# Performance work log

Hardware: AMD Instinct MI355X
Metric: run time of the kernel (lower is better)

## Reference

```python
import jax, jax.numpy as jnp
import numpy as np

N = 4096
NHID = 256
K1, K2, K3 = 3072, 2304, 1728


def _layernorm(x, g, b, eps=1e-5):
    m = jnp.mean(x, axis=-1, keepdims=True)
    v = jnp.mean((x - m) ** 2, axis=-1, keepdims=True)
    return (x - m) / jnp.sqrt(v + eps) * g + b


def _gcn(x, A, W, b):
    # PyG GCNConv: add self loops, symmetric norm D^-1/2 (A+I) D^-1/2,
    # messages flow row(source) -> col(target): out[j] = sum_i Anorm[i,j] (xW)[i] + b
    n = A.shape[0]
    A_sl = A + jnp.eye(n, dtype=A.dtype)
    deg = A_sl.sum(0)  # in-degree over col index incl. self loop
    dinv = jnp.where(deg > 0, deg ** -0.5, 0.0)
    An = A_sl * dinv[:, None] * dinv[None, :]
    return An.T @ (x @ W) + b


def _sagpool(x, A, Wp, bp, k):
    score = jnp.tanh(_gcn(x, A, Wp, bp)[:, 0])  # [n]
    vals, perm = jax.lax.top_k(score, k)
    x_new = x[perm] * vals[:, None]
    A_new = A[perm][:, perm]  # induced subgraph of directed edges
    return x_new, A_new


def _readout(x):
    # cat([global_max_pool, global_mean_pool]) for a single graph -> [1, 2*nhid]
    return jnp.concatenate([x.max(0), x.mean(0)])[None, :]


def setup_inputs() -> dict:
    key = jax.random.key(0)
    ks = jax.random.split(key, 10)
    s = 0.05
    return {
        'feature': jax.random.normal(ks[0], (N, 500), jnp.float32),
        'img_info': jax.random.normal(ks[1], (N, 6), jnp.float32),
        'Wp': jax.random.normal(ks[2], (6, 12), jnp.float32) * s,
        'bp': jnp.zeros((12,), jnp.float32),
        'ln_f_g': jnp.ones((500,), jnp.float32),
        'ln_f_b': jnp.zeros((500,), jnp.float32),
        'ln_p_g': jnp.ones((12,), jnp.float32),
        'ln_p_b': jnp.zeros((12,), jnp.float32),
        'W1': jax.random.normal(ks[3], (512, NHID), jnp.float32) * s,
        'b1': jnp.zeros((NHID,), jnp.float32),
        'Wpool1': jax.random.normal(ks[4], (NHID, 1), jnp.float32) * s,
        'bpool1': jnp.zeros((1,), jnp.float32),
        'W2': jax.random.normal(ks[5], (NHID, NHID), jnp.float32) * s,
        'b2': jnp.zeros((NHID,), jnp.float32),
        'Wpool2': jax.random.normal(ks[6], (NHID, 1), jnp.float32) * s,
        'bpool2': jnp.zeros((1,), jnp.float32),
        'W3': jax.random.normal(ks[7], (NHID, NHID), jnp.float32) * s,
        'b3': jnp.zeros((NHID,), jnp.float32),
        'Wpool3': jax.random.normal(ks[8], (NHID, 1), jnp.float32) * s,
        'bpool3': jnp.zeros((1,), jnp.float32),
    }


def reference(feature, img_info, Wp, bp, ln_f_g, ln_f_b, ln_p_g, ln_p_b,
              W1, b1, Wpool1, bpool1, W2, b2, Wpool2, bpool2,
              W3, b3, Wpool3, bpool3):
    # pos embedding + self-attention over nodes
    pos = img_info @ Wp + bp                                  # [N,12]
    att = jax.nn.softmax(pos @ pos.T / jnp.sqrt(12.0), axis=1)  # [N,N]
    pos = att @ pos

    f = _layernorm(feature, ln_f_g, ln_f_b)
    p = _layernorm(pos, ln_p_g, ln_p_b)
    x0 = jnp.concatenate([f, p], axis=1)                      # [N,512]

    # edge construction: upper-triangular directed edges where sqdist < 0.5*max sqdist
    sq = jnp.sum(x0 * x0, axis=1)
    d2 = sq[:, None] - 2.0 * (x0 @ x0.T) + sq[None, :]        # [N,N]
    t = 0.5 * d2.max()
    n = x0.shape[0]
    iu = jnp.triu(jnp.ones((n, n), bool), 1)
    A = jnp.where((d2 < t) & iu, 1.0, 0.0).astype(x0.dtype)

    x = jax.nn.relu(_gcn(x0, A, W1, b1))
    x, A = _sagpool(x, A, Wpool1, bpool1, K1)
    x1 = _readout(x)

    x = jax.nn.relu(_gcn(x, A, W2, b2))
    x, A = _sagpool(x, A, Wpool2, bpool2, K2)
    x2 = _readout(x)

    x = jax.nn.relu(_gcn(x, A, W3, b3))
    x, A = _sagpool(x, A, Wpool3, bpool3, K3)
    x3 = _readout(x)

    return x1 + x2 + x3  # [1, 512]
```

## Files before the change

### kernel.cpp

```cpp
#include <hip/hip_runtime.h>
#include <math.h>

#define NN 4096
#define RB 128

typedef __attribute__((ext_vector_type(8))) short bf16x8;
typedef __attribute__((ext_vector_type(4))) float f32x4;

__device__ __forceinline__ unsigned encf(float f) {
  unsigned u = __float_as_uint(f);
  return (u & 0x80000000u) ? ~u : (u | 0x80000000u);
}
__device__ __forceinline__ float decf(unsigned u) {
  return __uint_as_float((u & 0x80000000u) ? (u ^ 0x80000000u) : ~u);
}
__device__ __forceinline__ unsigned short f2bf(float f) {
  unsigned u = __float_as_uint(f);
  return (unsigned short)((u + 0x7fffu + ((u >> 16) & 1u)) >> 16);
}

__global__ void k_pos(const float* img, const float* Wp, const float* bp, float* pos,
                      float* out, unsigned* dmax) {
  if (blockIdx.x == 0) {
    int tt = threadIdx.x;
    out[tt] = 0.f; out[256 + tt] = 0.f;
    if (tt == 0) *dmax = 0u;
  }
  int t = blockIdx.x * 256 + threadIdx.x;
  if (t >= NN * 12) return;
  int i = t / 12, d = t % 12;
  float s = bp[d];
#pragma unroll
  for (int k = 0; k < 6; ++k) s += img[i * 6 + k] * Wp[k * 12 + d];
  pos[t] = s;
}

__global__ __launch_bounds__(256) void k_attn3(const float* pos, float* out) {
  __shared__ float sp[12][256];
  int t = threadIdx.x, lane = t & 63, w = t >> 6;
  int ib = blockIdx.x * 8 + w * 2;
  float pi[2][12];
#pragma unroll
  for (int r = 0; r < 2; ++r)
#pragma unroll
    for (int d = 0; d < 12; ++d) pi[r][d] = pos[(ib + r) * 12 + d] * 0.28867513459481287f;
  float sl[2] = {0.f, 0.f};
  float acc[2][12] = {};
  const float4* p4 = (const float4*)pos;
  for (int kt = 0; kt < NN; kt += 256) {
    __syncthreads();
    int j = kt + t;
    float4 a = p4[j * 3 + 0], b = p4[j * 3 + 1], c = p4[j * 3 + 2];
    sp[0][t] = a.x; sp[1][t] = a.y; sp[2][t] = a.z; sp[3][t] = a.w;
    sp[4][t] = b.x; sp[5][t] = b.y; sp[6][t] = b.z; sp[7][t] = b.w;
    sp[8][t] = c.x; sp[9][t] = c.y; sp[10][t] = c.z; sp[11][t] = c.w;
    __syncthreads();
#pragma unroll
    for (int q = 0; q < 4; ++q) {
      int jj = q * 64 + lane;
      float pj[12];
#pragma unroll
      for (int d = 0; d < 12; ++d) pj[d] = sp[d][jj];
#pragma unroll
      for (int r = 0; r < 2; ++r) {
        float s = 0.f;
#pragma unroll
        for (int d = 0; d < 12; ++d) s = fmaf(pi[r][d], pj[d], s);
        float e = __expf(s);
        sl[r] += e;
#pragma unroll
        for (int d = 0; d < 12; ++d) acc[r][d] = fmaf(e, pj[d], acc[r][d]);
      }
    }
  }
#pragma unroll
  for (int r = 0; r < 2; ++r) {
    float s = sl[r];
#pragma unroll
    for (int o = 32; o > 0; o >>= 1) s += __shfl_xor(s, o);
    float ad[12];
#pragma unroll
    for (int d = 0; d < 12; ++d) {
      ad[d] = acc[r][d];
#pragma unroll
      for (int o = 32; o > 0; o >>= 1) ad[d] += __shfl_xor(ad[d], o);
    }
    if (lane == 0) {
      float inv = 1.f / s;
#pragma unroll
      for (int d = 0; d < 12; ++d) out[(ib + r) * 12 + d] = ad[d] * inv;
    }
  }
}

__global__ __launch_bounds__(256) void k_lnx(const float* f, const float* g, const float* b,
                                             const float* p, const float* pg, const float* pb,
                                             float* x0, unsigned short* x0h, float* sqv,
                                             int* degA) {
  __shared__ float row[512];
  __shared__ float wrA[4], wrB[4], wrC[4];
  int i = blockIdx.x, t = threadIdx.x, lane = t & 63, w = t >> 6;
  if (t == 0) degA[i] = 0;
  float v1 = f[i * 500 + t];
  float v2 = (t < 244) ? f[i * 500 + 256 + t] : 0.f;
  float part = v1 + v2;
#pragma unroll
  for (int o = 32; o > 0; o >>= 1) part += __shfl_xor(part, o);
  if (lane == 0) wrA[w] = part;
  __syncthreads();
  float m = (wrA[0] + wrA[1] + wrA[2] + wrA[3]) * (1.f / 500.f);
  float d1 = v1 - m, d2 = v2 - m;
  float pvv = d1 * d1 + ((t < 244) ? d2 * d2 : 0.f);
#pragma unroll
  for (int o = 32; o > 0; o >>= 1) pvv += __shfl_xor(pvv, o);
  if (lane == 0) wrB[w] = pvv;
  __syncthreads();
  float scale = 1.f / sqrtf((wrB[0] + wrB[1] + wrB[2] + wrB[3]) * (1.f / 500.f) + 1e-5f);
  row[t] = d1 * scale * g[t] + b[t];
  if (t < 244) row[256 + t] = d2 * scale * g[256 + t] + b[256 + t];
  if (t >= 244) {
    int tt = t - 244;
    float pv[12], pm = 0.f;
#pragma unroll
    for (int d = 0; d < 12; ++d) { pv[d] = p[i * 12 + d]; pm += pv[d]; }
    pm *= (1.f / 12.f);
    float pvar = 0.f;
#pragma unroll
    for (int d = 0; d < 12; ++d) { float dd = pv[d] - pm; pvar += dd * dd; }
    pvar *= (1.f / 12.f);
    float ps = 1.f / sqrtf(pvar + 1e-5f);
    row[500 + tt] = (pv[tt] - pm) * ps * pg[tt] + pb[tt];
  }
  __syncthreads();
  float a = row[t], c = row[256 + t];
  float sq = a * a + c * c;
#pragma unroll
  for (int o = 32; o > 0; o >>= 1) sq += __shfl_xor(sq, o);
  if (lane == 0) wrC[w] = sq;
  __syncthreads();
  if (t == 0) sqv[i] = wrC[0] + wrC[1] + wrC[2] + wrC[3];
  x0[(size_t)i * 512 + t] = a;
  x0[(size_t)i * 512 + 256 + t] = c;
  x0h[(size_t)i * 512 + t] = f2bf(a);
  x0h[(size_t)i * 512 + 256 + t] = f2bf(c);
}

#define BK 64
template <bool MASK>
__global__ __launch_bounds__(256) void k_d2m(const unsigned short* X, const float* sqv,
                                             unsigned* dmax, float* tileMin,
                                             unsigned char* ATm, int* deg) {
  __shared__ unsigned short As[2][128 * BK];
  __shared__ unsigned short Bs[2][128 * BK];
  __shared__ float wmax[4], wmin[4];
  const int NT = NN / 128;
  int bid0 = blockIdx.x;
  int bid = (bid0 & 7) * 66 + (bid0 >> 3);
  int ti = 0, rem = bid;
  while (rem >= NT - ti) { rem -= NT - ti; ++ti; }
  int tj = ti + rem;
  int t = threadIdx.x, lane = t & 63, w = t >> 6;
  int wr = w >> 1, wc = w & 1;
  const unsigned short* Abase = X + (size_t)ti * 128 * 512;
  const unsigned short* Bbase = X + (size_t)tj * 128 * 512;
  int lr = lane >> 3, lc = lane & 7;

  float thr = 0.f;
  if (MASK) {
    thr = 0.5f * decf(*dmax);
    uint4 z = make_uint4(0u, 0u, 0u, 0u);
    if (ti != tj) {
#pragma unroll
      for (int q0 = 0; q0 < 4; ++q0) {
        int q = t + q0 * 256; int r = q >> 3, c4 = q & 7;
        *(uint4*)(ATm + (size_t)(ti * 128 + r) * NN + tj * 128 + c4 * 16) = z;
      }
    }
    if (tileMin[blockIdx.x] >= thr) {
#pragma unroll
      for (int q0 = 0; q0 < 4; ++q0) {
        int q = t + q0 * 256; int r = q >> 3, c4 = q & 7;
        *(uint4*)(ATm + (size_t)(tj * 128 + r) * NN + ti * 128 + c4 * 16) = z;
      }
      return;
    }
  }

  auto stage = [&](int buf, int k0) {
#pragma unroll
    for (int i = 0; i < 4; ++i) {
      int q = w * 4 + i;
      int r = q * 8 + lr;
      int cs = lc ^ (r & 7);
      __builtin_amdgcn_global_load_lds(
          (const __attribute__((address_space(1))) unsigned int*)(Abase + (size_t)r * 512 + k0 + cs * 8),
          (__attribute__((address_space(3))) unsigned int*)(&As[buf][q * 512]), 16, 0, 0);
      __builtin_amdgcn_global_load_lds(
          (const __attribute__((address_space(1))) unsigned int*)(Bbase + (size_t)r * 512 + k0 + cs * 8),
          (__attribute__((address_space(3))) unsigned int*)(&Bs[buf][q * 512]), 16, 0, 0);
    }
  };

  stage(0, 0);

  f32x4 acc[4][4] = {};
  int rl = lane & 15, kg = lane >> 4;
  for (int step = 0; step < 8; ++step) {
    int cur = step & 1;
    if (step < 7) {
      stage(cur ^ 1, (step + 1) * BK);
      asm volatile("s_waitcnt vmcnt(8)" ::: "memory");
    } else {
      asm volatile("s_waitcnt vmcnt(0)" ::: "memory");
    }
    __builtin_amdgcn_sched_barrier(0);
    __builtin_amdgcn_s_barrier();
#pragma unroll
    for (int ks = 0; ks < 2; ++ks) {
      bf16x8 af[4], bq[4];
#pragma unroll
      for (int f = 0; f < 4; ++f) {
        int rA = wr * 64 + f * 16 + rl;
        af[f] = *(const bf16x8*)(&As[cur][rA * BK + (((ks * 4 + kg) ^ (rA & 7)) << 3)]);
        int rB = wc * 64 + f * 16 + rl;
        bq[f] = *(const bf16x8*)(&Bs[cur][rB * BK + (((ks * 4 + kg) ^ (rB & 7)) << 3)]);
      }
#pragma unroll
      for (int a = 0; a < 4; ++a)
#pragma unroll
        for (int b = 0; b < 4; ++b)
          acc[a][b] = __builtin_amdgcn_mfma_f32_16x16x32_bf16(af[a], bq[b], acc[a][b], 0, 0, 0);
    }
    __builtin_amdgcn_sched_barrier(0);
    __builtin_amdgcn_s_barrier();
  }
  int rbase = ti * 128 + wr * 64 + ((lane >> 4) << 2);
  int cbase = tj * 128 + wc * 64 + (lane & 15);
  if (!MASK) {
    float lm = -1e30f, lmin = 1e30f;
#pragma unroll
    for (int a = 0; a < 4; ++a) {
      float si[4];
#pragma unroll
      for (int r = 0; r < 4; ++r) si[r] = sqv[rbase + a * 16 + r];
#pragma unroll
      for (int b = 0; b < 4; ++b) {
        int gj = cbase + b * 16;
        float sj = sqv[gj];
#pragma unroll
        for (int r = 0; r < 4; ++r) {
          float d2v = si[r] - 2.f * acc[a][b][r] + sj;
          lm = fmaxf(lm, d2v);
          if (rbase + a * 16 + r < gj) lmin = fminf(lmin, d2v);
        }
      }
    }
#pragma unroll
    for (int o = 32; o > 0; o >>= 1) {
      lm = fmaxf(lm, __shfl_xor(lm, o));
      lmin = fminf(lmin, __shfl_xor(lmin, o));
    }
    if (lane == 0) { wmax[w] = lm; wmin[w] = lmin; }
    __syncthreads();
    if (t == 0) {
      atomicMax(dmax, encf(fmaxf(fmaxf(wmax[0], wmax[1]), fmaxf(wmax[2], wmax[3]))));
      tileMin[blockIdx.x] = fminf(fminf(wmin[0], wmin[1]), fminf(wmin[2], wmin[3]));
    }
  } else {
#pragma unroll
    for (int b = 0; b < 4; ++b) {
      int gj = cbase + b * 16;
      float sj = sqv[gj];
      int rowcnt = 0;
#pragma unroll
      for (int a = 0; a < 4; ++a) {
        int gi0 = rbase + a * 16;
        union { unsigned char c[4]; unsigned u; } m4;
#pragma unroll
        for (int r = 0; r < 4; ++r) {
          float d2v = sqv[gi0 + r] - 2.f * acc[a][b][r] + sj;
          unsigned char mv = (d2v < thr && (gi0 + r) < gj) ? 1 : 0;
          m4.c[r] = mv; rowcnt += mv;
        }
        *(unsigned*)(ATm + (size_t)gj * NN + gi0) = m4.u;
      }
      if (rowcnt) atomicAdd(&deg[gj], rowcnt);
    }
  }
}

__global__ __launch_bounds__(256) void k_gemm(const float* A, const float* B, const int* deg,
                                              float* C, int M, int N, int K) {
  __shared__ float Ast[16][34];
  __shared__ float Bs[16][64];
  int t = threadIdx.x, tx = t & 15, ty = t >> 4;
  int nbx = N >> 6;
  int total = gridDim.x;
  int bid0 = blockIdx.x;
  int bid = (bid0 & 7) * (total >> 3) + (bid0 >> 3);
  int m0 = (bid / nbx) * 32, n0 = (bid % nbx) * 64;
  int ar = t >> 3, ac = (t * 2) & 15;
  int br = t >> 4, bc = (t & 15) * 4;
  float2 ra = *(const float2*)(A + (size_t)(m0 + ar) * K + ac);
  float4 rb = *(const float4*)(B + (size_t)br * N + n0 + bc);
  float acc[2][4] = {};
  for (int k0 = 0; k0 < K; k0 += 16) {
    Ast[ac][ar] = ra.x; Ast[ac + 1][ar] = ra.y;
    *(float4*)(&Bs[br][bc]) = rb;
    __syncthreads();
    if (k0 + 16 < K) {
      ra = *(const float2*)(A + (size_t)(m0 + ar) * K + k0 + 16 + ac);
      rb = *(const float4*)(B + (size_t)(k0 + 16 + br) * N + n0 + bc);
    }
#pragma unroll
    for (int kk = 0; kk < 16; ++kk) {
      float2 av = *(const float2*)(&Ast[kk][ty * 2]);
      float4 bv = *(const float4*)(&Bs[kk][tx * 4]);
      acc[0][0] = fmaf(av.x, bv.x, acc[0][0]);
      acc[0][1] = fmaf(av.x, bv.y, acc[0][1]);
      acc[0][2] = fmaf(av.x, bv.z, acc[0][2]);
      acc[0][3] = fmaf(av.x, bv.w, acc[0][3]);
      acc[1][0] = fmaf(av.y, bv.x, acc[1][0]);
      acc[1][1] = fmaf(av.y, bv.y, acc[1][1]);
      acc[1][2] = fmaf(av.y, bv.z, acc[1][2]);
      acc[1][3] = fmaf(av.y, bv.w, acc[1][3]);
    }
    __syncthreads();
  }
#pragma unroll
  for (int a = 0; a < 2; ++a) {
    float dv = 1.f / sqrtf((float)(1 + deg[m0 + ty * 2 + a]));
#pragma unroll
    for (int b2 = 0; b2 < 4; ++b2)
      C[(size_t)(m0 + ty * 2 + a) * N + n0 + tx * 4 + b2] = acc[a][b2] * dv;
  }
}

__global__ __launch_bounds__(256) void k_agg(const float* y, const unsigned char* ATm,
                                             const int* deg, const float* bias,
                                             const float* Wpool, float* out, float* y2, int n) {
  __shared__ unsigned char mrow[256];
  __shared__ int s_any;
  __shared__ float wred[4];
  int j = blockIdx.x, t = threadIdx.x, lane = t & 63, w = t >> 6;
  int dg = deg[j];
  float dj = 1.f / sqrtf((float)(1 + dg));
  float acc = y[(size_t)j * 256 + t];
  if (dg != 0) {
    for (int i0 = 0; i0 < n; i0 += 256) {
      if (t == 0) s_any = 0;
      __syncthreads();
      unsigned char m = ATm[(size_t)j * n + i0 + t];
      mrow[t] = m;
      if (m) s_any = 1;
      __syncthreads();
      if (s_any) {
        for (int u = 0; u < 256; ++u)
          if (mrow[u]) acc += y[(size_t)(i0 + u) * 256 + t];
      }
      __syncthreads();
    }
  }
  float o = fmaxf(dj * acc + bias[t], 0.f);
  out[(size_t)j * 256 + t] = o;
  float rv = o * Wpool[t];
#pragma unroll
  for (int os = 32; os > 0; os >>= 1) rv += __shfl_xor(rv, os);
  if (lane == 0) wred[w] = rv;
  __syncthreads();
  if (t == 0) y2[j] = dj * (wred[0] + wred[1] + wred[2] + wred[3]);
}

__global__ __launch_bounds__(256) void k_scorek(const float* y2, const unsigned char* ATm,
                                                const int* deg, const float* bp,
                                                float* score, int n) {
  int w = threadIdx.x >> 6, lane = threadIdx.x & 63;
  int j = blockIdx.x * 4 + w;
  if (j >= n) return;
  int dg = deg[j];
  float dj = 1.f / sqrtf((float)(1 + dg));
  float s = 0.f;
  if (dg != 0) {
    const uint4* row = (const uint4*)(ATm + (size_t)j * n);
    for (int p = lane; p < n / 16; p += 64) {
      uint4 v = row[p];
      if (v.x | v.y | v.z | v.w) {
        int base = p * 16;
#pragma unroll
        for (int q = 0; q < 4; ++q) {
          unsigned u = (&v.x)[q];
#pragma unroll
          for (int b2 = 0; b2 < 4; ++b2)
            if ((u >> (8 * b2)) & 0xffu) s += y2[base + q * 4 + b2];
        }
      }
    }
    for (int sh = 32; sh > 0; sh >>= 1) s += __shfl_down(s, sh);
  }
  if (lane == 0) score[j] = tanhf(dj * (y2[j] + s) + bp[0]);
}

__global__ __launch_bounds__(1024) void k_topsel(const float* score, int n, int k,
                                                 int* perm, float* vals) {
  __shared__ unsigned keys[4096];
  __shared__ unsigned hist[256];
  __shared__ unsigned s_state[2];
  __shared__ unsigned woff[16];
  int t = threadIdx.x, lane = t & 63, w = t >> 6;
  for (int i = t; i < 4096; i += 1024) keys[i] = (i < n) ? encf(score[i]) : 0u;
  if (t == 0) { s_state[0] = 0u; s_state[1] = (unsigned)k; }
  __syncthreads();

  for (int pass = 0; pass < 4; ++pass) {
    int shift = 24 - pass * 8;
    if (t < 256) hist[t] = 0u;
    __syncthreads();
    unsigned prefix = s_state[0];
    unsigned need = s_state[1];
    unsigned pmask = pass ? (0xFFFFFFFFu << (shift + 8)) : 0u;
    for (int i = t; i < n; i += 1024) {
      unsigned kk = keys[i];
      if ((kk & pmask) == prefix) atomicAdd(&hist[(kk >> shift) & 255u], 1u);
    }
    __syncthreads();
    if (w == 0) {
      unsigned h[4], suf[4];
#pragma unroll
      for (int r = 0; r < 4; ++r) h[r] = hist[lane * 4 + r];
      suf[3] = h[3]; suf[2] = h[2] + suf[3]; suf[1] = h[1] + suf[2]; suf[0] = h[0] + suf[1];
      unsigned lsum = suf[0];
      unsigned s = lsum;
#pragma unroll
      for (int off = 1; off < 64; off <<= 1) {
        unsigned o = __shfl_down(s, off);
        if (lane + off < 64) s += o;
      }
      unsigned Hl = s - lsum;
      int cand = -1; unsigned cumAt = 0, histAt = 0;
#pragma unroll
      for (int r = 0; r < 4; ++r) {
        unsigned c = Hl + suf[r];
        if (c >= need) { cand = lane * 4 + r; cumAt = c; histAt = h[r]; }
      }
      int gmax = cand;
#pragma unroll
      for (int off = 32; off > 0; off >>= 1) {
        int o = __shfl_xor(gmax, off);
        gmax = o > gmax ? o : gmax;
      }
      if (cand == gmax && cand >= 0) {
        s_state[0] = prefix | ((unsigned)cand << shift);
        s_state[1] = need - (cumAt - histAt);
      }
    }
    __syncthreads();
  }
  unsigned cutoff = s_state[0];
  unsigned tcount = s_state[1];
  unsigned G = (unsigned)k - tcount;

  int i0 = t * 4;
  unsigned loc[4], cnt = 0;
#pragma unroll
  for (int r = 0; r < 4; ++r) {
    unsigned kk = keys[i0 + r];
    unsigned g = (kk > cutoff) ? 1u : 0u;
    unsigned e = (kk == cutoff) ? 1u : 0u;
    loc[r] = cnt;
    cnt += (g << 16) | e;
  }
  unsigned inc = cnt;
#pragma unroll
  for (int off = 1; off < 64; off <<= 1) {
    unsigned o = __shfl_up(inc, off);
    if (lane >= off) inc += o;
  }
  if (lane == 63) woff[w] = inc;
  __syncthreads();
  if (t == 0) {
    unsigned run = 0;
    for (int q = 0; q < 16; ++q) { unsigned v = woff[q]; woff[q] = run; run += v; }
  }
  __syncthreads();
  unsigned base = woff[w] + (inc - cnt);
#pragma unroll
  for (int r = 0; r < 4; ++r) {
    unsigned kk = keys[i0 + r];
    unsigned p = base + loc[r];
    if (kk > cutoff) {
      unsigned pos = p >> 16;
      perm[pos] = i0 + r; vals[pos] = decf(kk);
    } else if (kk == cutoff) {
      unsigned pe = p & 0xffffu;
      if (pe < tcount) { perm[G + pe] = i0 + r; vals[G + pe] = decf(kk); }
    }
  }
}

__global__ __launch_bounds__(256) void k_gxp(const float* xg, const int* perm, const float* vals,
                                             float* xp, float* pmax, float* psum, int k) {
  int b = blockIdx.x, t = threadIdx.x;
  float m = -1e30f, s = 0.f;
  for (int r = b; r < k; r += RB) {
    float v = xg[(size_t)perm[r] * 256 + t] * vals[r];
    xp[(size_t)r * 256 + t] = v;
    m = fmaxf(m, v); s += v;
  }
  pmax[b * 256 + t] = m; psum[b * 256 + t] = s;
}
__global__ void k_rfin(const float* pmax, const float* psum, float* out, int k) {
  int t = threadIdx.x;
  float m = -1e30f, s = 0.f;
  for (int q = 0; q < RB; ++q) { m = fmaxf(m, pmax[q * 256 + t]); s += psum[q * 256 + t]; }
  out[t] += m;
  out[256 + t] += s / (float)k;
}

__global__ __launch_bounds__(256) void k_gatherA(const unsigned char* ATold, const int* perm,
                                                 const int* degCur,
                                                 unsigned char* ATnew, int* degNext,
                                                 int nold, int kn) {
  __shared__ int sperm[4096];
  __shared__ int redi[256];
  int t = threadIdx.x, c = blockIdx.x;
  for (int r = t; r < kn; r += 256) sperm[r] = perm[r];
  __syncthreads();
  int src = sperm[c];
  unsigned char* orow = ATnew + (size_t)c * kn;
  if (degCur[src] == 0) {
    uint4 z = make_uint4(0u, 0u, 0u, 0u);
    for (int r = t; r < kn / 16; r += 256) ((uint4*)orow)[r] = z;
    if (t == 0) degNext[c] = 0;
    return;
  }
  const unsigned char* row = ATold + (size_t)src * nold;
  int cnt = 0;
  for (int r = t; r < kn; r += 256) { unsigned char v = row[sperm[r]]; orow[r] = v; cnt += v; }
  redi[t] = cnt; __syncthreads();
  for (int s = 128; s > 0; s >>= 1) { if (t < s) redi[t] += redi[t + s]; __syncthreads(); }
  if (t == 0) degNext[c] = redi[0];
}

static void run_layer(hipStream_t stream, const float* x_in, int n, int inC,
                      const float* W, const float* b, const float* Wpool, const float* bpool,
                      int k, const unsigned char* ATcur, unsigned char* ATnext,
                      const int* degCur, int* degNext,
                      float* ybuf, float* xg, float* xp, float* y2,
                      float* score, int* perm, float* vals, float* pmax, float* psum, float* out) {
  k_gemm<<<(n / 32) * 4, 256, 0, stream>>>(x_in, W, degCur, ybuf, n, 256, inC);
  k_agg<<<n, 256, 0, stream>>>(ybuf, ATcur, degCur, b, Wpool, xg, y2, n);
  k_scorek<<<n / 4, 256, 0, stream>>>(y2, ATcur, degCur, bpool, score, n);
  k_topsel<<<1, 1024, 0, stream>>>(score, n, k, perm, vals);
  k_gxp<<<RB, 256, 0, stream>>>(xg, perm, vals, xp, pmax, psum, k);
  k_rfin<<<1, 256, 0, stream>>>(pmax, psum, out, k);
  if (ATnext) k_gatherA<<<k, 256, 0, stream>>>(ATcur, perm, degCur, ATnext, degNext, n, k);
}

extern "C" void kernel_launch(void* const* d_in, const int* in_sizes, int n_in,
                              void* d_out, int out_size, void* d_ws, size_t ws_size,
                              hipStream_t stream) {
  const float* feature = (const float*)d_in[0];
  const float* img     = (const float*)d_in[1];
  const float* Wp      = (const float*)d_in[2];
  const float* bp      = (const float*)d_in[3];
  const float* ln_f_g  = (const float*)d_in[4];
  const float* ln_f_b  = (const float*)d_in[5];
  const float* ln_p_g  = (const float*)d_in[6];
  const float* ln_p_b  = (const float*)d_in[7];
  const float* W1 = (const float*)d_in[8];   const float* b1 = (const float*)d_in[9];
  const float* Wpool1 = (const float*)d_in[10]; const float* bpool1 = (const float*)d_in[11];
  const float* W2 = (const float*)d_in[12];  const float* b2 = (const float*)d_in[13];
  const float* Wpool2 = (const float*)d_in[14]; const float* bpool2 = (const float*)d_in[15];
  const float* W3 = (const float*)d_in[16];  const float* b3 = (const float*)d_in[17];
  const float* Wpool3 = (const float*)d_in[18]; const float* bpool3 = (const float*)d_in[19];
  float* out = (float*)d_out;
  (void)in_sizes; (void)n_in; (void)out_size; (void)ws_size;

  char* w = (char*)d_ws;
  size_t off = 0;
  auto alloc = [&](size_t bytes) -> char* {
    off = (off + 255) & ~(size_t)255;
    char* p = w + off;
    off += bytes;
    return p;
  };
  float* pos0 = (float*)alloc((size_t)NN * 12 * 4);
  float* pos1 = (float*)alloc((size_t)NN * 12 * 4);
  float* x0   = (float*)alloc((size_t)NN * 512 * 4);
  unsigned short* x0h = (unsigned short*)alloc((size_t)NN * 512 * 2);
  float* sqv  = (float*)alloc((size_t)NN * 4);
  unsigned* dmax = (unsigned*)alloc(4);
  float* tileMin = (float*)alloc(528 * 4);
  int* degA = (int*)alloc((size_t)NN * 4);
  int* degB = (int*)alloc((size_t)NN * 4);
  float* ybuf = (float*)alloc((size_t)NN * 256 * 4);
  float* xg   = (float*)alloc((size_t)NN * 256 * 4);
  float* xp   = (float*)alloc((size_t)NN * 256 * 4);
  float* y2   = (float*)alloc((size_t)NN * 4);
  float* score= (float*)alloc((size_t)NN * 4);
  int*   perm = (int*)alloc((size_t)NN * 4);
  float* vals = (float*)alloc((size_t)NN * 4);
  float* pmax = (float*)alloc(RB * 256 * 4);
  float* psum = (float*)alloc(RB * 256 * 4);
  unsigned char* ATa = (unsigned char*)alloc((size_t)NN * NN);
  unsigned char* ATb = (unsigned char*)alloc((size_t)3072 * 3072);

  k_pos<<<(NN * 12 + 255) / 256, 256, 0, stream>>>(img, Wp, bp, pos0, out, dmax);
  k_attn3<<<NN / 8, 256, 0, stream>>>(pos0, pos1);
  k_lnx<<<NN, 256, 0, stream>>>(feature, ln_f_g, ln_f_b, pos1, ln_p_g, ln_p_b,
                                x0, x0h, sqv, degA);

  const int NT = NN / 128, TT = NT * (NT + 1) / 2;
  k_d2m<false><<<TT, 256, 0, stream>>>(x0h, sqv, dmax, tileMin, nullptr, nullptr);
  k_d2m<true><<<TT, 256, 0, stream>>>(x0h, sqv, dmax, tileMin, ATa, degA);

  run_layer(stream, x0, 4096, 512, W1, b1, Wpool1, bpool1, 3072, ATa, ATb, degA, degB,
            ybuf, xg, xp, y2, score, perm, vals, pmax, psum, out);
  run_layer(stream, xp, 3072, 256, W2, b2, Wpool2, bpool2, 2304, ATb, ATa, degB, degA,
            ybuf, xg, xp, y2, score, perm, vals, pmax, psum, out);
  run_layer(stream, xp, 2304, 256, W3, b3, Wpool3, bpool3, 1728, ATa, nullptr, degA, nullptr,
            ybuf, xg, xp, y2, score, perm, vals, pmax, psum, out);
}
```

Before: 231.9 us.

## Fuse pooling gather with adjacency gather and defer readout reduction

The feature gather/readout-partial kernel and the adjacency-subgraph gather kernel are merged into one launch, with block ranges split by role. The three per-layer readout finalize kernels are replaced by one final kernel that reduces all three layers' partials using separate buffers, so out no longer needs zeroing in k_pos. It also raises wave priority around the MFMA loop in the distance GEMM. The goal is fewer kernel launches and serialization points, at the cost of extra partial buffers.

After: 217.4 us. 1.07x faster.

```diff
diff --git a/kernel.cpp b/kernel.cpp
--- a/kernel.cpp
+++ b/kernel.cpp
@@ -20,12 +20,8 @@
 }
 
 __global__ void k_pos(const float* img, const float* Wp, const float* bp, float* pos,
-                      float* out, unsigned* dmax) {
-  if (blockIdx.x == 0) {
-    int tt = threadIdx.x;
-    out[tt] = 0.f; out[256 + tt] = 0.f;
-    if (tt == 0) *dmax = 0u;
-  }
+                      unsigned* dmax) {
+  if (blockIdx.x == 0 && threadIdx.x == 0) *dmax = 0u;
   int t = blockIdx.x * 256 + threadIdx.x;
   if (t >= NN * 12) return;
   int i = t / 12, d = t % 12;
@@ -215,6 +211,7 @@
     }
     __builtin_amdgcn_sched_barrier(0);
     __builtin_amdgcn_s_barrier();
+    __builtin_amdgcn_s_setprio(1);
 #pragma unroll
     for (int ks = 0; ks < 2; ++ks) {
       bf16x8 af[4], bq[4];
@@ -231,6 +228,7 @@
         for (int b = 0; b < 4; ++b)
           acc[a][b] = __builtin_amdgcn_mfma_f32_16x16x32_bf16(af[a], bq[b], acc[a][b], 0, 0, 0);
     }
+    __builtin_amdgcn_s_setprio(0);
     __builtin_amdgcn_sched_barrier(0);
     __builtin_amdgcn_s_barrier();
   }
@@ -497,48 +495,54 @@
   }
 }
 
-__global__ __launch_bounds__(256) void k_gxp(const float* xg, const int* perm, const float* vals,
-                                             float* xp, float* pmax, float* psum, int k) {
-  int b = blockIdx.x, t = threadIdx.x;
-  float m = -1e30f, s = 0.f;
-  for (int r = b; r < k; r += RB) {
-    float v = xg[(size_t)perm[r] * 256 + t] * vals[r];
-    xp[(size_t)r * 256 + t] = v;
-    m = fmaxf(m, v); s += v;
-  }
-  pmax[b * 256 + t] = m; psum[b * 256 + t] = s;
-}
-__global__ void k_rfin(const float* pmax, const float* psum, float* out, int k) {
-  int t = threadIdx.x;
-  float m = -1e30f, s = 0.f;
-  for (int q = 0; q < RB; ++q) { m = fmaxf(m, pmax[q * 256 + t]); s += psum[q * 256 + t]; }
-  out[t] += m;
-  out[256 + t] += s / (float)k;
-}
-
-__global__ __launch_bounds__(256) void k_gatherA(const unsigned char* ATold, const int* perm,
-                                                 const int* degCur,
-                                                 unsigned char* ATnew, int* degNext,
-                                                 int nold, int kn) {
+__global__ __launch_bounds__(256) void k_pool(const float* xg, const int* perm, const float* vals,
+                                              float* xp, float* pmax, float* psum, int k,
+                                              const unsigned char* ATold, const int* degCur,
+                                              unsigned char* ATnew, int* degNext, int nold) {
   __shared__ int sperm[4096];
   __shared__ int redi[256];
-  int t = threadIdx.x, c = blockIdx.x;
-  for (int r = t; r < kn; r += 256) sperm[r] = perm[r];
+  int b = blockIdx.x, t = threadIdx.x;
+  if (b < RB) {
+    float m = -1e30f, s = 0.f;
+    for (int r = b; r < k; r += RB) {
+      float v = xg[(size_t)perm[r] * 256 + t] * vals[r];
+      xp[(size_t)r * 256 + t] = v;
+      m = fmaxf(m, v); s += v;
+    }
+    pmax[b * 256 + t] = m; psum[b * 256 + t] = s;
+    return;
+  }
+  int c = b - RB;
+  for (int r = t; r < k; r += 256) sperm[r] = perm[r];
   __syncthreads();
   int src = sperm[c];
-  unsigned char* orow = ATnew + (size_t)c * kn;
+  unsigned char* orow = ATnew + (size_t)c * k;
   if (degCur[src] == 0) {
     uint4 z = make_uint4(0u, 0u, 0u, 0u);
-    for (int r = t; r < kn / 16; r += 256) ((uint4*)orow)[r] = z;
+    for (int r = t; r < k / 16; r += 256) ((uint4*)orow)[r] = z;
     if (t == 0) degNext[c] = 0;
     return;
   }
   const unsigned char* row = ATold + (size_t)src * nold;
   int cnt = 0;
-  for (int r = t; r < kn; r += 256) { unsigned char v = row[sperm[r]]; orow[r] = v; cnt += v; }
+  for (int r = t; r < k; r += 256) { unsigned char v = row[sperm[r]]; orow[r] = v; cnt += v; }
   redi[t] = cnt; __syncthreads();
   for (int s = 128; s > 0; s >>= 1) { if (t < s) redi[t] += redi[t + s]; __syncthreads(); }
   if (t == 0) degNext[c] = redi[0];
+}
+
+__global__ void k_rfin3(const float* pm0, const float* ps0, int k0,
+                        const float* pm1, const float* ps1, int k1,
+                        const float* pm2, const float* ps2, int k2, float* out) {
+  int t = threadIdx.x;
+  float m0 = -1e30f, s0 = 0.f, m1 = -1e30f, s1 = 0.f, m2 = -1e30f, s2 = 0.f;
+  for (int q = 0; q < RB; ++q) {
+    m0 = fmaxf(m0, pm0[q * 256 + t]); s0 += ps0[q * 256 + t];
+    m1 = fmaxf(m1, pm1[q * 256 + t]); s1 += ps1[q * 256 + t];
+    m2 = fmaxf(m2, pm2[q * 256 + t]); s2 += ps2[q * 256 + t];
+  }
+  out[t] = m0 + m1 + m2;
+  out[256 + t] = s0 / (float)k0 + s1 / (float)k1 + s2 / (float)k2;
 }
 
 static void run_layer(hipStream_t stream, const float* x_in, int n, int inC,
@@ -546,14 +550,14 @@
                       int k, const unsigned char* ATcur, unsigned char* ATnext,
                       const int* degCur, int* degNext,
                       float* ybuf, float* xg, float* xp, float* y2,
-                      float* score, int* perm, float* vals, float* pmax, float* psum, float* out) {
+                      float* score, int* perm, float* vals, float* pmax, float* psum) {
   k_gemm<<<(n / 32) * 4, 256, 0, stream>>>(x_in, W, degCur, ybuf, n, 256, inC);
   k_agg<<<n, 256, 0, stream>>>(ybuf, ATcur, degCur, b, Wpool, xg, y2, n);
   k_scorek<<<n / 4, 256, 0, stream>>>(y2, ATcur, degCur, bpool, score, n);
   k_topsel<<<1, 1024, 0, stream>>>(score, n, k, perm, vals);
-  k_gxp<<<RB, 256, 0, stream>>>(xg, perm, vals, xp, pmax, psum, k);
-  k_rfin<<<1, 256, 0, stream>>>(pmax, psum, out, k);
-  if (ATnext) k_gatherA<<<k, 256, 0, stream>>>(ATcur, perm, degCur, ATnext, degNext, n, k);
+  int grid = RB + (ATnext ? k : 0);
+  k_pool<<<grid, 256, 0, stream>>>(xg, perm, vals, xp, pmax, psum, k,
+                                   ATcur, degCur, ATnext, degNext, n);
 }
 
 extern "C" void kernel_launch(void* const* d_in, const int* in_sizes, int n_in,
@@ -600,12 +604,16 @@
   float* score= (float*)alloc((size_t)NN * 4);
   int*   perm = (int*)alloc((size_t)NN * 4);
   float* vals = (float*)alloc((size_t)NN * 4);
-  float* pmax = (float*)alloc(RB * 256 * 4);
-  float* psum = (float*)alloc(RB * 256 * 4);
+  float* pmax0 = (float*)alloc(RB * 256 * 4);
+  float* psum0 = (float*)alloc(RB * 256 * 4);
+  float* pmax1 = (float*)alloc(RB * 256 * 4);
+  float* psum1 = (float*)alloc(RB * 256 * 4);
+  float* pmax2 = (float*)alloc(RB * 256 * 4);
+  float* psum2 = (float*)alloc(RB * 256 * 4);
   unsigned char* ATa = (unsigned char*)alloc((size_t)NN * NN);
   unsigned char* ATb = (unsigned char*)alloc((size_t)3072 * 3072);
 
-  k_pos<<<(NN * 12 + 255) / 256, 256, 0, stream>>>(img, Wp, bp, pos0, out, dmax);
+  k_pos<<<(NN * 12 + 255) / 256, 256, 0, stream>>>(img, Wp, bp, pos0, dmax);
   k_attn3<<<NN / 8, 256, 0, stream>>>(pos0, pos1);
   k_lnx<<<NN, 256, 0, stream>>>(feature, ln_f_g, ln_f_b, pos1, ln_p_g, ln_p_b,
                                 x0, x0h, sqv, degA);
@@ -615,9 +623,11 @@
   k_d2m<true><<<TT, 256, 0, stream>>>(x0h, sqv, dmax, tileMin, ATa, degA);
 
   run_layer(stream, x0, 4096, 512, W1, b1, Wpool1, bpool1, 3072, ATa, ATb, degA, degB,
-            ybuf, xg, xp, y2, score, perm, vals, pmax, psum, out);
+            ybuf, xg, xp, y2, score, perm, vals, pmax0, psum0);
   run_layer(stream, xp, 3072, 256, W2, b2, Wpool2, bpool2, 2304, ATb, ATa, degB, degA,
-            ybuf, xg, xp, y2, score, perm, vals, pmax, psum, out);
+            ybuf, xg, xp, y2, score, perm, vals, pmax1, psum1);
   run_layer(stream, xp, 2304, 256, W3, b3, Wpool3, bpool3, 1728, ATa, nullptr, degA, nullptr,
-            ybuf, xg, xp, y2, score, perm, vals, pmax, psum, out);
-}
+            ybuf, xg, xp, y2, score, perm, vals, pmax2, psum2);
+  k_rfin3<<<1, 256, 0, stream>>>(pmax0, psum0, 3072, pmax1, psum1, 2304,
+                                 pmax2, psum2, 1728, out);
+}
```
